# Kernel optimization log

Hardware: AMD Instinct MI355X
Metric: run time of the kernel (lower is better)

Reference implementation:

```python
import jax, jax.numpy as jnp
import numpy as np

PATCH_NUM = 196  # 14*14 patch grid
BASE_NUM = 128

def setup_inputs() -> dict:
    key = jax.random.key(0)
    k1, k2, k3, k4 = jax.random.split(key, 4)
    b = 128
    return {
        "h_scores": jax.random.normal(k1, (b, BASE_NUM, 3, 14), dtype=jnp.float32),
        "v_score": jax.random.normal(k2, (b, BASE_NUM, 3, 14), dtype=jnp.float32),
        "h_base": jax.random.normal(k3, (b, BASE_NUM, 16), dtype=jnp.float32),
        "v_base": jax.random.normal(k4, (b, BASE_NUM, 16), dtype=jnp.float32),
    }

def reference(h_scores, v_score, h_base, v_base):
    b = h_scores.shape[0]
    # base images per base vector: [b, k, m, n]
    base_matrix = jnp.einsum('bkn,bkm->bkmn', h_base, v_base)
    # per-patch, per-channel scores: [b, k, 3, n', m'] -> [b, k, 3, P]
    score = jnp.einsum('bkcn,bkcm->bkcnm', h_scores, v_score)
    score = score.reshape(b, BASE_NUM, 3, PATCH_NUM)
    # [b, P, 3, k]; softmax over base dim (matches per-patch F.softmax(dim=2))
    score = jnp.transpose(score, (0, 3, 2, 1))
    score = jax.nn.softmax(score, axis=-1)
    # weighted sum of base images: [b, P, 3, m, n]
    res = jnp.einsum('bpck,bkmn->bpcmn', score, base_matrix)
    return res
```

## Files before the change

### kernel.cpp

```cpp
#include <hip/hip_runtime.h>

typedef __attribute__((ext_vector_type(8))) short bf16x8;
typedef __attribute__((ext_vector_type(4))) float f32x4;

#define PATCHES 196
#define ROWS 588
#define NCHUNK 10
#define SCORE_B_STRIDE 5376

static __device__ __forceinline__ unsigned f2bf2(float a, float b) {
    union { float f; unsigned u; } x, y; x.f = a; y.f = b;
    unsigned lo = (x.u + 0x7FFFu + ((x.u >> 16) & 1u)) >> 16;
    unsigned hi = (y.u + 0x7FFFu + ((y.u >> 16) & 1u)) & 0xFFFF0000u;
    return lo | hi;
}

__global__ __launch_bounds__(256) void bm_build(
    const float* __restrict__ h_base,
    const float* __restrict__ v_base,
    unsigned short* __restrict__ bm)
{
    __shared__ float hb[2048], vb[2048];
    const int b = blockIdx.x, t = threadIdx.x;
    const float* hg = h_base + (size_t)b * 2048;
    const float* vg = v_base + (size_t)b * 2048;
#pragma unroll
    for (int i = 0; i < 8; ++i) { hb[i*256+t] = hg[i*256+t]; vb[i*256+t] = vg[i*256+t]; }
    __syncthreads();

    const int m = t >> 4, n = t & 15;
    unsigned short* dst = bm + (size_t)b * 32768 + t * 128;
#pragma unroll
    for (int k0 = 0; k0 < 128; k0 += 8) {
        float p[8];
#pragma unroll
        for (int j = 0; j < 8; ++j)
            p[j] = vb[(k0+j)*16 + m] * hb[(k0+j)*16 + n];
        uint4 u = { f2bf2(p[0],p[1]), f2bf2(p[2],p[3]), f2bf2(p[4],p[5]), f2bf2(p[6],p[7]) };
        *(uint4*)(dst + k0) = u;
    }
}

__global__ __launch_bounds__(256) void patch_gemm(
    const float* __restrict__ h_scores,
    const float* __restrict__ v_score,
    const unsigned short* __restrict__ bm,
    float* __restrict__ out)
{
    __shared__ __align__(16) char lds[81920];

    const int bid = blockIdx.x;
    const int xcd  = bid & 7;
    const int rest = bid >> 3;
    const int b     = (rest / NCHUNK) * 8 + xcd;
    const int chunk = rest % NCHUNK;
    const int t = threadIdx.x;

    const uint4* vsg = (const uint4*)(v_score + (size_t)b * SCORE_B_STRIDE);
    uint4* vsl = (uint4*)(lds + 16384);
#pragma unroll
    for (int i = 0; i < 6; ++i) { int ci = t + i*256; if (ci < 1344) vsl[ci] = vsg[ci]; }
    __syncthreads();

    {
        const int r = t >> 2, kq = t & 3;
        const int grow = chunk * 64 + r;
        const bool valid = grow < ROWS;
        const int p = grow / 3, c = grow - p * 3;
        const int np = p / 14, mp = p - np * 14;
        const float* vs_l = (const float*)(lds + 16384);
        const float* hsb  = h_scores + (size_t)b * SCORE_B_STRIDE;
        const int vix = c * 14 + mp;
        const int hix = c * 14 + np;

        float sc[32];
#pragma unroll
        for (int j = 0; j < 32; ++j) {
            const int k = kq * 32 + j;
            float hsv = valid ? hsb[k * 42 + hix] : 0.f;
            sc[j] = hsv * vs_l[k * 42 + vix];
        }
        float mx = sc[0];
#pragma unroll
        for (int j = 1; j < 32; ++j) mx = fmaxf(mx, sc[j]);
        mx = fmaxf(mx, __shfl_xor(mx, 1));
        mx = fmaxf(mx, __shfl_xor(mx, 2));
        float sum = 0.f;
#pragma unroll
        for (int j = 0; j < 32; ++j) { sc[j] = __expf(sc[j] - mx); sum += sc[j]; }
        sum += __shfl_xor(sum, 1);
        sum += __shfl_xor(sum, 2);
        const float inv = 1.f / sum;

        const int sw = (r & 7) << 4;
#pragma unroll
        for (int s2 = 0; s2 < 4; ++s2) {
            const int k0 = kq * 32 + s2 * 8;
            uint4 u = { f2bf2(sc[s2*8+0]*inv, sc[s2*8+1]*inv),
                        f2bf2(sc[s2*8+2]*inv, sc[s2*8+3]*inv),
                        f2bf2(sc[s2*8+4]*inv, sc[s2*8+5]*inv),
                        f2bf2(sc[s2*8+6]*inv, sc[s2*8+7]*inv) };
            *(uint4*)(lds + r * 256 + ((k0 * 2) ^ sw)) = u;
        }
    }
    __syncthreads();

    {
        const uint4* bmg = (const uint4*)(bm + (size_t)b * 32768);
#pragma unroll
        for (int i = 0; i < 16; ++i) {
            const int ci = t + i * 256;
            uint4 v = bmg[ci];
            const int mn = ci >> 4, kb = (ci & 15) * 16;
            *(uint4*)(lds + 16384 + mn * 256 + (kb ^ ((mn & 7) << 4))) = v;
        }
    }
    __syncthreads();

    const int w = t >> 6, lane = t & 63;
    const int wm = w >> 1, wn = w & 1;
    const int lr = lane & 15, lg = lane >> 4;

    bf16x8 afrag[2][4];
#pragma unroll
    for (int mi = 0; mi < 2; ++mi) {
        const int r2 = wm * 32 + mi * 16 + lr;
        const int sw = (r2 & 7) << 4;
#pragma unroll
        for (int kc = 0; kc < 4; ++kc)
            afrag[mi][kc] = *(const bf16x8*)(lds + r2 * 256 + ((kc * 64 + lg * 16) ^ sw));
    }

    f32x4 acc[2][8];
#pragma unroll
    for (int mi = 0; mi < 2; ++mi)
#pragma unroll
        for (int nt = 0; nt < 8; ++nt)
            acc[mi][nt] = (f32x4){0.f, 0.f, 0.f, 0.f};

#pragma unroll
    for (int nt = 0; nt < 8; ++nt) {
        const int mn = wn * 128 + nt * 16 + lr;
        const char* bmrow = lds + 16384 + mn * 256;
        const int sw = (mn & 7) << 4;
#pragma unroll
        for (int kc = 0; kc < 4; ++kc) {
            bf16x8 bfrag = *(const bf16x8*)(bmrow + ((kc * 64 + lg * 16) ^ sw));
            acc[0][nt] = __builtin_amdgcn_mfma_f32_16x16x32_bf16(afrag[0][kc], bfrag, acc[0][nt], 0, 0, 0);
            acc[1][nt] = __builtin_amdgcn_mfma_f32_16x16x32_bf16(afrag[1][kc], bfrag, acc[1][nt], 0, 0, 0);
        }
    }

    float* ob = out + (size_t)b * (ROWS * 256);
#pragma unroll
    for (int mi = 0; mi < 2; ++mi) {
        const int growo = chunk * 64 + wm * 32 + mi * 16 + lg * 4;
#pragma unroll
        for (int nt = 0; nt < 8; ++nt) {
            const int col = wn * 128 + nt * 16 + lr;
#pragma unroll
            for (int reg = 0; reg < 4; ++reg) {
                const int gr = growo + reg;
                if (gr < ROWS) ob[(size_t)gr * 256 + col] = acc[mi][nt][reg];
            }
        }
    }
}

extern "C" void kernel_launch(void* const* d_in, const int* in_sizes, int n_in,
                              void* d_out, int out_size, void* d_ws, size_t ws_size,
                              hipStream_t stream) {
    const float* h_scores = (const float*)d_in[0];
    const float* v_score  = (const float*)d_in[1];
    const float* h_base   = (const float*)d_in[2];
    const float* v_base   = (const float*)d_in[3];
    float* out = (float*)d_out;
    unsigned short* bm = (unsigned short*)d_ws;

    const int B = in_sizes[0] / SCORE_B_STRIDE;

    bm_build<<<B, 256, 0, stream>>>(h_base, v_base, bm);
    patch_gemm<<<B * NCHUNK, 256, 0, stream>>>(h_scores, v_score, bm, out);
}
```

Baseline: 38.08 us.

## Store base matrix in MFMA fragment order and read B operand directly from global

The base-matrix builder now writes bf16 products in a layout indexed by k-chunk and mn, so each MFMA lane can load its B fragment straight from global memory with coalesced 16-byte loads. This removes the per-block LDS staging of the 64KB base matrix and the v_score LDS copy, shrinking LDS from 80KB to 16KB so several blocks fit per CU (launch bounds set to 3). The builder is split across two blocks per batch with transposed shared arrays. The trade is that B fragments are read from L2/global inside the MFMA loop rather than from LDS, and out-of-range rows are clamped instead of zeroed.

```diff
diff --git a/kernel.cpp b/kernel.cpp
--- a/kernel.cpp
+++ b/kernel.cpp
@@ -18,67 +18,65 @@
 __global__ __launch_bounds__(256) void bm_build(
     const float* __restrict__ h_base,
     const float* __restrict__ v_base,
-    unsigned short* __restrict__ bm)
+    uint4* __restrict__ bmv)
 {
-    __shared__ float hb[2048], vb[2048];
-    const int b = blockIdx.x, t = threadIdx.x;
-    const float* hg = h_base + (size_t)b * 2048;
-    const float* vg = v_base + (size_t)b * 2048;
+    __shared__ float hbT[16][68];
+    __shared__ float vbT[16][68];
+    const int b = blockIdx.x, zb = blockIdx.y, t = threadIdx.x;
+    const float* hg = h_base + (size_t)b * 2048 + zb * 1024;
+    const float* vg = v_base + (size_t)b * 2048 + zb * 1024;
 #pragma unroll
-    for (int i = 0; i < 8; ++i) { hb[i*256+t] = hg[i*256+t]; vb[i*256+t] = vg[i*256+t]; }
+    for (int i = 0; i < 4; ++i) {
+        const int idx = t + i * 256;
+        hbT[idx & 15][idx >> 4] = hg[idx];
+        vbT[idx & 15][idx >> 4] = vg[idx];
+    }
     __syncthreads();
 
     const int m = t >> 4, n = t & 15;
-    unsigned short* dst = bm + (size_t)b * 32768 + t * 128;
+    uint4* dst = bmv + ((size_t)b * 16 + zb * 8) * 256 + t;
 #pragma unroll
-    for (int k0 = 0; k0 < 128; k0 += 8) {
+    for (int i = 0; i < 8; ++i) {
+        const float* vp = &vbT[m][i * 8];
+        const float* hp = &hbT[n][i * 8];
         float p[8];
 #pragma unroll
-        for (int j = 0; j < 8; ++j)
-            p[j] = vb[(k0+j)*16 + m] * hb[(k0+j)*16 + n];
-        uint4 u = { f2bf2(p[0],p[1]), f2bf2(p[2],p[3]), f2bf2(p[4],p[5]), f2bf2(p[6],p[7]) };
-        *(uint4*)(dst + k0) = u;
+        for (int j = 0; j < 8; ++j) p[j] = vp[j] * hp[j];
+        uint4 u = { f2bf2(p[0],p[1]), f2bf2(p[2],p[3]),
+                    f2bf2(p[4],p[5]), f2bf2(p[6],p[7]) };
+        dst[i * 256] = u;
     }
 }
 
-__global__ __launch_bounds__(256) void patch_gemm(
+__global__ __launch_bounds__(256, 3) void patch_gemm(
     const float* __restrict__ h_scores,
     const float* __restrict__ v_score,
-    const unsigned short* __restrict__ bm,
+    const uint4* __restrict__ bmv,
     float* __restrict__ out)
 {
-    __shared__ __align__(16) char lds[81920];
+    __shared__ __align__(16) char lds[16384];
 
     const int bid = blockIdx.x;
-    const int xcd  = bid & 7;
-    const int rest = bid >> 3;
-    const int b     = (rest / NCHUNK) * 8 + xcd;
+    const int xcd = bid & 7, rest = bid >> 3;
+    const int b = (rest / NCHUNK) * 8 + xcd;
     const int chunk = rest % NCHUNK;
     const int t = threadIdx.x;
-
-    const uint4* vsg = (const uint4*)(v_score + (size_t)b * SCORE_B_STRIDE);
-    uint4* vsl = (uint4*)(lds + 16384);
-#pragma unroll
-    for (int i = 0; i < 6; ++i) { int ci = t + i*256; if (ci < 1344) vsl[ci] = vsg[ci]; }
-    __syncthreads();
 
     {
         const int r = t >> 2, kq = t & 3;
         const int grow = chunk * 64 + r;
-        const bool valid = grow < ROWS;
-        const int p = grow / 3, c = grow - p * 3;
+        const int geff = grow < ROWS ? grow : ROWS - 1;
+        const int p = geff / 3, c = geff - p * 3;
         const int np = p / 14, mp = p - np * 14;
-        const float* vs_l = (const float*)(lds + 16384);
-        const float* hsb  = h_scores + (size_t)b * SCORE_B_STRIDE;
-        const int vix = c * 14 + mp;
-        const int hix = c * 14 + np;
+        const float* hsb = h_scores + (size_t)b * SCORE_B_STRIDE;
+        const float* vsb = v_score  + (size_t)b * SCORE_B_STRIDE;
+        const int hix = c * 14 + np, vix = c * 14 + mp;
 
         float sc[32];
 #pragma unroll
         for (int j = 0; j < 32; ++j) {
             const int k = kq * 32 + j;
-            float hsv = valid ? hsb[k * 42 + hix] : 0.f;
-            sc[j] = hsv * vs_l[k * 42 + vix];
+            sc[j] = hsb[k * 42 + hix] * vsb[k * 42 + vix];
         }
         float mx = sc[0];
 #pragma unroll
@@ -95,24 +93,12 @@
         const int sw = (r & 7) << 4;
 #pragma unroll
         for (int s2 = 0; s2 < 4; ++s2) {
-            const int k0 = kq * 32 + s2 * 8;
+            const int kpos = (kq * 32 + s2 * 8) * 2;
             uint4 u = { f2bf2(sc[s2*8+0]*inv, sc[s2*8+1]*inv),
                         f2bf2(sc[s2*8+2]*inv, sc[s2*8+3]*inv),
                         f2bf2(sc[s2*8+4]*inv, sc[s2*8+5]*inv),
                         f2bf2(sc[s2*8+6]*inv, sc[s2*8+7]*inv) };
-            *(uint4*)(lds + r * 256 + ((k0 * 2) ^ sw)) = u;
-        }
-    }
-    __syncthreads();
-
-    {
-        const uint4* bmg = (const uint4*)(bm + (size_t)b * 32768);
-#pragma unroll
-        for (int i = 0; i < 16; ++i) {
-            const int ci = t + i * 256;
-            uint4 v = bmg[ci];
-            const int mn = ci >> 4, kb = (ci & 15) * 16;
-            *(uint4*)(lds + 16384 + mn * 256 + (kb ^ ((mn & 7) << 4))) = v;
+            *(uint4*)(lds + r * 256 + (kpos ^ sw)) = u;
         }
     }
     __syncthreads();
@@ -131,6 +117,8 @@
             afrag[mi][kc] = *(const bf16x8*)(lds + r2 * 256 + ((kc * 64 + lg * 16) ^ sw));
     }
 
+    const uint4* bmb = bmv + (size_t)b * 4096;
+
     f32x4 acc[2][8];
 #pragma unroll
     for (int mi = 0; mi < 2; ++mi)
@@ -141,11 +129,10 @@
 #pragma unroll
     for (int nt = 0; nt < 8; ++nt) {
         const int mn = wn * 128 + nt * 16 + lr;
-        const char* bmrow = lds + 16384 + mn * 256;
-        const int sw = (mn & 7) << 4;
 #pragma unroll
         for (int kc = 0; kc < 4; ++kc) {
-            bf16x8 bfrag = *(const bf16x8*)(bmrow + ((kc * 64 + lg * 16) ^ sw));
+            uint4 raw = bmb[(kc * 4 + lg) * 256 + mn];
+            bf16x8 bfrag = *(bf16x8*)&raw;
             acc[0][nt] = __builtin_amdgcn_mfma_f32_16x16x32_bf16(afrag[0][kc], bfrag, acc[0][nt], 0, 0, 0);
             acc[1][nt] = __builtin_amdgcn_mfma_f32_16x16x32_bf16(afrag[1][kc], bfrag, acc[1][nt], 0, 0, 0);
         }
@@ -175,10 +162,10 @@
     const float* h_base   = (const float*)d_in[2];
     const float* v_base   = (const float*)d_in[3];
     float* out = (float*)d_out;
-    unsigned short* bm = (unsigned short*)d_ws;
+    uint4* bmv = (uint4*)d_ws;
 
     const int B = in_sizes[0] / SCORE_B_STRIDE;
 
-    bm_build<<<B, 256, 0, stream>>>(h_base, v_base, bm);
-    patch_gemm<<<B * NCHUNK, 256, 0, stream>>>(h_scores, v_score, bm, out);
+    bm_build<<<dim3(B, 2), 256, 0, stream>>>(h_base, v_base, bmv);
+    patch_gemm<<<B * NCHUNK, 256, 0, stream>>>(h_scores, v_score, bmv, out);
 }
```

Measured after the change: 35.07 us. -7.9%, faster.
